# Kernel optimization log

Measured on AMD Instinct MI355X. Metric: run time of the kernel, lower is better.

Reference implementation:

```python
import jax, jax.numpy as jnp
import numpy as np

N = 100000
E = 3200000
IN_C = 128
HID = 128
OUT_C = 1


def setup_inputs() -> dict:
    key = jax.random.key(0)
    ks = jax.random.split(key, 12)
    x = jax.random.normal(ks[0], (N, IN_C), dtype=jnp.float32)
    edge_index = jax.random.randint(ks[1], (2, E), 0, N, dtype=jnp.int64)
    # GCNConv weights (PyG: lin(x) then aggregate, plus bias)
    s1 = 1.0 / np.sqrt(IN_C)
    s2 = 1.0 / np.sqrt(HID)
    W1 = jax.random.uniform(ks[2], (IN_C, HID), jnp.float32, -s1, s1)
    b1 = jnp.zeros((HID,), jnp.float32)
    W2 = jax.random.uniform(ks[3], (HID, HID), jnp.float32, -s2, s2)
    b2 = jnp.zeros((HID,), jnp.float32)
    sl1 = 1.0 / np.sqrt(2 * HID + IN_C)
    Wl1 = jax.random.uniform(ks[4], (2 * HID + IN_C, HID), jnp.float32, -sl1, sl1)
    bl1 = jax.random.uniform(ks[5], (HID,), jnp.float32, -sl1, sl1)
    Wl2 = jax.random.uniform(ks[6], (HID, OUT_C), jnp.float32, -s2, s2)
    bl2 = jax.random.uniform(ks[7], (OUT_C,), jnp.float32, -s2, s2)
    return {"x": x, "edge_index": edge_index, "W1": W1, "b1": b1,
            "W2": W2, "b2": b2, "Wl1": Wl1, "bl1": bl1, "Wl2": Wl2, "bl2": bl2}


def _gcn_conv(x, W, b, row, col, deg_inv_sqrt):
    # GCNConv: D^{-1/2} (A + I) D^{-1/2} X W + b  (self-loops added with weight 1)
    xw = x @ W                                   # [N, H]
    norm = deg_inv_sqrt[row] * deg_inv_sqrt[col] # [E]
    msg = xw[row] * norm[:, None]                # gather + scale
    agg = jax.ops.segment_sum(msg, col, num_segments=x.shape[0])  # scatter-add
    agg = agg + xw * (deg_inv_sqrt * deg_inv_sqrt)[:, None]       # self-loop term
    return agg + b


def reference(x, edge_index, W1, b1, W2, b2, Wl1, bl1, Wl2, bl2):
    row, col = edge_index[0], edge_index[1]  # source -> target
    n = x.shape[0]
    # degree with self-loops (edge weight 1)
    deg = jax.ops.segment_sum(jnp.ones_like(col, dtype=x.dtype), col, num_segments=n) + 1.0
    deg_inv_sqrt = jax.lax.rsqrt(deg)
    x1 = jax.nn.relu(_gcn_conv(x, W1, b1, row, col, deg_inv_sqrt))
    # dropout is identity in eval mode
    x2 = jax.nn.relu(_gcn_conv(x1, W2, b2, row, col, deg_inv_sqrt))
    h = jnp.concatenate([x, x1, x2], axis=-1)   # [N, in + 2*hidden]
    h = jax.nn.relu(h @ Wl1 + bl1)
    out = jax.nn.sigmoid(h @ Wl2 + bl2)         # [N, 1]
    return out
```

## Files before the change

kernel.cpp:

```cpp
#include <hip/hip_runtime.h>
#include <hip/hip_fp16.h>
#include <math.h>


typedef __attribute__((ext_vector_type(8))) short bf16x8;
typedef __attribute__((ext_vector_type(4))) float f32x4;

#define BSHIFT 5
#define NB 64
#define MAXBUK 4096

__global__ __launch_bounds__(1024) void k_bhist(const int* __restrict__ col,
                                                int* __restrict__ partials,
                                                int nbuk, int e) {
    __shared__ int h[MAXBUK];
    int tid = threadIdx.x;
    for (int i = tid; i < nbuk; i += 1024) h[i] = 0;
    __syncthreads();
    for (long long i = (long long)blockIdx.x * 1024 + tid; i < e;
         i += (long long)NB * 1024)
        atomicAdd(&h[col[i] >> BSHIFT], 1);
    __syncthreads();
    for (int i = tid; i < nbuk; i += 1024)
        partials[(size_t)blockIdx.x * nbuk + i] = h[i];
}

__global__ __launch_bounds__(256) void k_bscan(int* __restrict__ partials,
                                               int* __restrict__ tot, int nbuk) {
    int gid = blockIdx.x * 256 + threadIdx.x;
    int w = gid >> 6, l = gid & 63;
    if (w >= nbuk) return;
    size_t idx = (size_t)l * nbuk + w;
    int v = partials[idx];
    int s = v;
    for (int d = 1; d < 64; d <<= 1) {
        int t = __shfl_up(s, d);
        if (l >= d) s += t;
    }
    partials[idx] = s - v;
    if (l == 63) tot[w] = s;
}

__global__ __launch_bounds__(256) void k_btot(const int* __restrict__ tot,
                                              int* __restrict__ base,
                                              int nbuk, int e) {
    __shared__ int s[256];
    __shared__ int carry_s;
    int t = threadIdx.x;
    if (t == 0) carry_s = 0;
    __syncthreads();
    for (int bb = 0; bb < nbuk; bb += 256) {
        int v = (bb + t < nbuk) ? tot[bb + t] : 0;
        s[t] = v;
        __syncthreads();
        for (int d = 1; d < 256; d <<= 1) {
            int a = (t >= d) ? s[t - d] : 0;
            __syncthreads();
            s[t] += a;
            __syncthreads();
        }
        int c0 = carry_s;
        if (bb + t < nbuk) base[bb + t] = s[t] - v + c0;
        __syncthreads();
        if (t == 0) carry_s = c0 + s[255];
        __syncthreads();
    }
    if (t == 0) base[nbuk] = e;
}

__global__ __launch_bounds__(1024) void k_bscatter(
    const int* __restrict__ row, const int* __restrict__ col,
    const int* __restrict__ base, const int* __restrict__ partials,
    int* __restrict__ bpack, int nbuk, int e) {
    __shared__ int cur[MAXBUK];
    int tid = threadIdx.x;
    for (int i = tid; i < nbuk; i += 1024)
        cur[i] = base[i] + partials[(size_t)blockIdx.x * nbuk + i];
    __syncthreads();
    for (long long i = (long long)blockIdx.x * 1024 + tid; i < e;
         i += (long long)NB * 1024) {
        int c = col[i];
        int pos = atomicAdd(&cur[c >> BSHIFT], 1);
        bpack[pos] = (row[i] << BSHIFT) | (c & 31);
    }
}

__global__ __launch_bounds__(256) void k_bfill(
    const int* __restrict__ bpack, const int* __restrict__ base,
    int* __restrict__ offs, int* __restrict__ srow,
    float* __restrict__ dinv, int n, int e, int nbuk) {
    __shared__ int h[32];
    __shared__ int cur[32];
    int b = blockIdx.x, tid = threadIdx.x;
    int nodeb = b << BSHIFT;
    if (tid < 32) h[tid] = 0;
    __syncthreads();
    int s0 = base[b], s1 = base[b + 1];
    for (int i = s0 + tid; i < s1; i += 256) atomicAdd(&h[bpack[i] & 31], 1);
    __syncthreads();
    if (tid < 32) {
        int v = h[tid];
        int s = v;
        for (int d = 1; d < 32; d <<= 1) {
            int t = __shfl_up(s, d);
            if (tid >= d) s += t;
        }
        int myoff = s0 + s - v;
        cur[tid] = myoff;
        int node = nodeb + tid;
        if (node < n) {
            offs[node] = myoff;
            dinv[node] = rsqrtf((float)v + 1.0f);
        }
    }
    if (b == nbuk - 1 && tid == 0) offs[n] = e;
    __syncthreads();
    for (int i = s0 + tid; i < s1; i += 256) {
        int p = bpack[i];
        int pos = atomicAdd(&cur[p & 31], 1);
        srow[pos] = p >> BSHIFT;
    }
}

__global__ void k_prep_w(const float* __restrict__ W1, const float* __restrict__ W2,
                         const float* __restrict__ Wl1, short* __restrict__ wb) {
    int i = blockIdx.x * blockDim.x + threadIdx.x;
    if (i >= 5 * 16384) return;
    int blk = i >> 14, rem = i & 16383;
    int k = rem >> 7, n = rem & 127;
    float v;
    if (blk == 0) v = W1[rem];
    else if (blk == 1) v = W2[rem];
    else v = Wl1[((blk - 2) * 128 + k) * 128 + n];
    unsigned u = __float_as_uint(v);
    unsigned hb = u & 0xFFFF0000u;
    float lo = v - __uint_as_float(hb);
    unsigned lb = __float_as_uint(lo);
    int kk = k >> 5, km = k & 31;
    int half = km >> 4, kq = km & 15, g = kq >> 2, j = kq & 3;
    int nt = n >> 4, c = n & 15;
    size_t idx = ((size_t)(kk * 8 + nt) * 64 + (g * 16 + c)) * 8 + (half * 4 + j);
    size_t base = (size_t)blk * 32768;
    wb[base + idx] = (short)(hb >> 16);
    wb[base + 16384 + idx] = (short)(lb >> 16);
}

__device__ inline short2 split_f(float x) {
    unsigned u = __float_as_uint(x);
    unsigned hb = u & 0xFFFF0000u;
    short h = (short)(u >> 16);
    short l = (short)(__float_as_uint(x - __uint_as_float(hb)) >> 16);
    return make_short2(h, l);
}

__global__ __launch_bounds__(256) void k_gemm_mfma(
    const float* __restrict__ src0, const float* __restrict__ src1,
    const float* __restrict__ src2, const short* __restrict__ wb,
    const float* __restrict__ dscale, const float* __restrict__ bias,
    const float* __restrict__ wl2, const float* __restrict__ bl2,
    void* __restrict__ Y, int n, int nkb, int mode) {
    __shared__ short wl[32768];
    int tid = threadIdx.x;
    int wave = tid >> 6, lane = tid & 63;
    int g = lane >> 4, c = lane & 15;
    int base = blockIdx.x * 128 + wave * 32;

    f32x4 acc[2][8];
#pragma unroll
    for (int a = 0; a < 2; ++a)
#pragma unroll
        for (int b = 0; b < 8; ++b) acc[a][b] = (f32x4){0.f, 0.f, 0.f, 0.f};

    for (int kb = 0; kb < nkb; ++kb) {
        const float* src = (kb == 0) ? src0 : ((kb == 1) ? src1 : src2);
        __syncthreads();
        {
            const int4* s = (const int4*)(wb + (size_t)kb * 32768);
            int4* d = (int4*)wl;
            for (int it = tid; it < 4096; it += 256) d[it] = s[it];
        }
        __syncthreads();
#pragma unroll
        for (int kk = 0; kk < 4; ++kk) {
            bf16x8 ah[2], al[2];
#pragma unroll
            for (int mf = 0; mf < 2; ++mf) {
                int node = base + mf * 16 + c;
                if (node >= n) node = n - 1;
                const float* p = src + (size_t)node * 128 + kk * 32 + g * 4;
                float4 v0 = *(const float4*)p;
                float4 v1 = *(const float4*)(p + 16);
                short2 s;
                s = split_f(v0.x); ah[mf][0] = s.x; al[mf][0] = s.y;
                s = split_f(v0.y); ah[mf][1] = s.x; al[mf][1] = s.y;
                s = split_f(v0.z); ah[mf][2] = s.x; al[mf][2] = s.y;
                s = split_f(v0.w); ah[mf][3] = s.x; al[mf][3] = s.y;
                s = split_f(v1.x); ah[mf][4] = s.x; al[mf][4] = s.y;
                s = split_f(v1.y); ah[mf][5] = s.x; al[mf][5] = s.y;
                s = split_f(v1.z); ah[mf][6] = s.x; al[mf][6] = s.y;
                s = split_f(v1.w); ah[mf][7] = s.x; al[mf][7] = s.y;
            }
#pragma unroll
            for (int nt = 0; nt < 8; ++nt) {
                int bidx = ((kk * 8 + nt) * 64 + lane) * 8;
                bf16x8 bh = *(const bf16x8*)&wl[bidx];
                bf16x8 bl = *(const bf16x8*)&wl[16384 + bidx];
#pragma unroll
                for (int mf = 0; mf < 2; ++mf) {
                    acc[mf][nt] = __builtin_amdgcn_mfma_f32_16x16x32_bf16(ah[mf], bh, acc[mf][nt], 0, 0, 0);
                    acc[mf][nt] = __builtin_amdgcn_mfma_f32_16x16x32_bf16(ah[mf], bl, acc[mf][nt], 0, 0, 0);
                    acc[mf][nt] = __builtin_amdgcn_mfma_f32_16x16x32_bf16(al[mf], bh, acc[mf][nt], 0, 0, 0);
                }
            }
        }
    }

    if (mode == 0) {
        __half* Yh = (__half*)Y;
#pragma unroll
        for (int mf = 0; mf < 2; ++mf) {
#pragma unroll
            for (int j = 0; j < 4; ++j) {
                int node = base + mf * 16 + g * 4 + j;
                if (node >= n) continue;
                float s = dscale[node];
#pragma unroll
                for (int nt = 0; nt < 8; ++nt)
                    Yh[(size_t)node * 128 + nt * 16 + c] =
                        __float2half(acc[mf][nt][j] * s);
            }
        }
    } else {
        float* Yf = (float*)Y;
        float wv[8], bv[8];
#pragma unroll
        for (int nt = 0; nt < 8; ++nt) {
            wv[nt] = wl2[nt * 16 + c];
            bv[nt] = bias[nt * 16 + c];
        }
        float blv = bl2[0];
#pragma unroll
        for (int mf = 0; mf < 2; ++mf) {
#pragma unroll
            for (int j = 0; j < 4; ++j) {
                float partial = 0.f;
#pragma unroll
                for (int nt = 0; nt < 8; ++nt)
                    partial += fmaxf(acc[mf][nt][j] + bv[nt], 0.f) * wv[nt];
#pragma unroll
                for (int m = 1; m < 16; m <<= 1) partial += __shfl_xor(partial, m);
                int node = base + mf * 16 + g * 4 + j;
                if (c == 0 && node < n)
                    Yf[node] = 1.f / (1.f + expf(-(partial + blv)));
            }
        }
    }
}

__global__ __launch_bounds__(256) void k_aggregate(
    const __half* __restrict__ xws, const float* __restrict__ dinv,
    const float* __restrict__ bias, const int* __restrict__ offs,
    const int* __restrict__ srow, float* __restrict__ out, int n) {
    long long t = (long long)blockIdx.x * blockDim.x + threadIdx.x;
    int node = (int)(t >> 6);
    int l = (int)t & 63;
    if (node >= n) return;
    int start = offs[node], end = offs[node + 1];
    const __half* xb = xws + l * 2;
    float2 acc = __half22float2(*(const __half2*)(xb + (size_t)node * 128));
    int e = start;
    for (; e + 7 < end; e += 8) {
        int r0 = srow[e],     r1 = srow[e + 1], r2 = srow[e + 2], r3 = srow[e + 3];
        int r4 = srow[e + 4], r5 = srow[e + 5], r6 = srow[e + 6], r7 = srow[e + 7];
        float2 v0 = __half22float2(*(const __half2*)(xb + (size_t)r0 * 128));
        float2 v1 = __half22float2(*(const __half2*)(xb + (size_t)r1 * 128));
        float2 v2 = __half22float2(*(const __half2*)(xb + (size_t)r2 * 128));
        float2 v3 = __half22float2(*(const __half2*)(xb + (size_t)r3 * 128));
        float2 v4 = __half22float2(*(const __half2*)(xb + (size_t)r4 * 128));
        float2 v5 = __half22float2(*(const __half2*)(xb + (size_t)r5 * 128));
        float2 v6 = __half22float2(*(const __half2*)(xb + (size_t)r6 * 128));
        float2 v7 = __half22float2(*(const __half2*)(xb + (size_t)r7 * 128));
        acc.x += ((v0.x + v1.x) + (v2.x + v3.x)) + ((v4.x + v5.x) + (v6.x + v7.x));
        acc.y += ((v0.y + v1.y) + (v2.y + v3.y)) + ((v4.y + v5.y) + (v6.y + v7.y));
    }
    for (; e < end; ++e) {
        float2 v = __half22float2(*(const __half2*)(xb + (size_t)srow[e] * 128));
        acc.x += v.x;
        acc.y += v.y;
    }
    float s = dinv[node];
    float2 b = *(const float2*)(bias + l * 2);
    acc.x = fmaxf(fmaf(acc.x, s, b.x), 0.f);
    acc.y = fmaxf(fmaf(acc.y, s, b.y), 0.f);
    *(float2*)(out + (size_t)node * 128 + l * 2) = acc;
}

extern "C" void kernel_launch(void* const* d_in, const int* in_sizes, int n_in,
                              void* d_out, int out_size, void* d_ws, size_t ws_size,
                              hipStream_t stream) {
    const float* x   = (const float*)d_in[0];
    const int*   ei  = (const int*)d_in[1];
    const float* W1  = (const float*)d_in[2];
    const float* b1  = (const float*)d_in[3];
    const float* W2  = (const float*)d_in[4];
    const float* b2  = (const float*)d_in[5];
    const float* Wl1 = (const float*)d_in[6];
    const float* bl1 = (const float*)d_in[7];
    const float* Wl2 = (const float*)d_in[8];
    const float* bl2 = (const float*)d_in[9];
    float* out = (float*)d_out;

    const int N = in_sizes[0] / 128;
    const int E = in_sizes[1] / 2;
    const int* row = ei;
    const int* col = ei + E;
    const int nbuk = (N + 31) >> 5;

    char* ws = (char*)d_ws;
    size_t off = 0;
    auto alloc = [&](size_t bytes) {
        void* p = ws + off;
        off += (bytes + 255) & ~(size_t)255;
        return p;
    };
    float*  dinv     = (float*)alloc((size_t)N * 4);
    int*    partials = (int*)alloc((size_t)NB * nbuk * 4);
    int*    tot      = (int*)alloc((size_t)nbuk * 4);
    int*    base     = (int*)alloc((size_t)(nbuk + 1) * 4);
    int*    offs     = (int*)alloc((size_t)(N + 1) * 4);
    int*    bpack    = (int*)alloc((size_t)E * 4);
    int*    srow     = (int*)alloc((size_t)E * 4);
    short*  wb       = (short*)alloc((size_t)5 * 32768 * 2);
    __half* bufA     = (__half*)alloc((size_t)N * 128 * 2);
    float*  bufB     = (float*)alloc((size_t)N * 128 * 4);
    float*  bufC     = (float*)alloc((size_t)N * 128 * 4);

    const int B = 256;
    int gG = (N + 127) / 128;
    int gP = (5 * 16384 + B - 1) / B;
    int gS = (nbuk * 64 + B - 1) / B;
    int gA = (int)(((long long)N * 64 + B - 1) / B);

    k_prep_w<<<gP, B, 0, stream>>>(W1, W2, Wl1, wb);
    k_bhist<<<NB, 1024, 0, stream>>>(col, partials, nbuk, E);
    k_bscan<<<gS, B, 0, stream>>>(partials, tot, nbuk);
    k_btot<<<1, B, 0, stream>>>(tot, base, nbuk, E);
    k_bscatter<<<NB, 1024, 0, stream>>>(row, col, base, partials, bpack, nbuk, E);
    k_bfill<<<nbuk, B, 0, stream>>>(bpack, base, offs, srow, dinv, N, E, nbuk);

    k_gemm_mfma<<<gG, B, 0, stream>>>(x, nullptr, nullptr, wb,
                                      dinv, nullptr, nullptr, nullptr,
                                      bufA, N, 1, 0);
    k_aggregate<<<gA, B, 0, stream>>>(bufA, dinv, b1, offs, srow, bufB, N);

    k_gemm_mfma<<<gG, B, 0, stream>>>(bufB, nullptr, nullptr, wb + 32768,
                                      dinv, nullptr, nullptr, nullptr,
                                      bufA, N, 1, 0);
    k_aggregate<<<gA, B, 0, stream>>>(bufA, dinv, b2, offs, srow, bufC, N);

    k_gemm_mfma<<<gG, B, 0, stream>>>(x, bufB, bufC, wb + 2 * 32768,
                                      nullptr, bl1, Wl2, bl2,
                                      out, N, 3, 1);
}
```

Measured before the change: 470.3 us.

## Store hidden activations x1,x2 in fp16 and unroll aggregation by 16

```diff
diff --git a/kernel.cpp b/kernel.cpp
--- a/kernel.cpp
+++ b/kernel.cpp
@@ -153,12 +153,34 @@
     return make_short2(h, l);
 }
 
+__device__ inline void loadA8(const void* src, int f16, size_t node, int off,
+                              float* v) {
+    if (f16) {
+        const __half* p = (const __half*)src + node * 128 + off;
+        int2 a = *(const int2*)p;
+        int2 b = *(const int2*)(p + 16);
+        const __half2* ah = (const __half2*)&a;
+        const __half2* bh = (const __half2*)&b;
+        float2 f;
+        f = __half22float2(ah[0]); v[0] = f.x; v[1] = f.y;
+        f = __half22float2(ah[1]); v[2] = f.x; v[3] = f.y;
+        f = __half22float2(bh[0]); v[4] = f.x; v[5] = f.y;
+        f = __half22float2(bh[1]); v[6] = f.x; v[7] = f.y;
+    } else {
+        const float* p = (const float*)src + node * 128 + off;
+        float4 v0 = *(const float4*)p;
+        float4 v1 = *(const float4*)(p + 16);
+        v[0] = v0.x; v[1] = v0.y; v[2] = v0.z; v[3] = v0.w;
+        v[4] = v1.x; v[5] = v1.y; v[6] = v1.z; v[7] = v1.w;
+    }
+}
+
 __global__ __launch_bounds__(256) void k_gemm_mfma(
-    const float* __restrict__ src0, const float* __restrict__ src1,
-    const float* __restrict__ src2, const short* __restrict__ wb,
+    const void* __restrict__ src0, const void* __restrict__ src1,
+    const void* __restrict__ src2, const short* __restrict__ wb,
     const float* __restrict__ dscale, const float* __restrict__ bias,
     const float* __restrict__ wl2, const float* __restrict__ bl2,
-    void* __restrict__ Y, int n, int nkb, int mode) {
+    void* __restrict__ Y, int n, int nkb, int mode, int f16mask) {
     __shared__ short wl[32768];
     int tid = threadIdx.x;
     int wave = tid >> 6, lane = tid & 63;
@@ -172,7 +194,8 @@
         for (int b = 0; b < 8; ++b) acc[a][b] = (f32x4){0.f, 0.f, 0.f, 0.f};
 
     for (int kb = 0; kb < nkb; ++kb) {
-        const float* src = (kb == 0) ? src0 : ((kb == 1) ? src1 : src2);
+        const void* src = (kb == 0) ? src0 : ((kb == 1) ? src1 : src2);
+        int f16 = (f16mask >> kb) & 1;
         __syncthreads();
         {
             const int4* s = (const int4*)(wb + (size_t)kb * 32768);
@@ -187,18 +210,15 @@
             for (int mf = 0; mf < 2; ++mf) {
                 int node = base + mf * 16 + c;
                 if (node >= n) node = n - 1;
-                const float* p = src + (size_t)node * 128 + kk * 32 + g * 4;
-                float4 v0 = *(const float4*)p;
-                float4 v1 = *(const float4*)(p + 16);
+                float v[8];
+                loadA8(src, f16, (size_t)node, kk * 32 + g * 4, v);
                 short2 s;
-                s = split_f(v0.x); ah[mf][0] = s.x; al[mf][0] = s.y;
-                s = split_f(v0.y); ah[mf][1] = s.x; al[mf][1] = s.y;
-                s = split_f(v0.z); ah[mf][2] = s.x; al[mf][2] = s.y;
-                s = split_f(v0.w); ah[mf][3] = s.x; al[mf][3] = s.y;
-                s = split_f(v1.x); ah[mf][4] = s.x; al[mf][4] = s.y;
-                s = split_f(v1.y); ah[mf][5] = s.x; al[mf][5] = s.y;
-                s = split_f(v1.z); ah[mf][6] = s.x; al[mf][6] = s.y;
-                s = split_f(v1.w); ah[mf][7] = s.x; al[mf][7] = s.y;
+#pragma unroll
+                for (int q = 0; q < 8; ++q) {
+                    s = split_f(v[q]);
+                    ah[mf][q] = s.x;
+                    al[mf][q] = s.y;
+                }
             }
 #pragma unroll
             for (int nt = 0; nt < 8; ++nt) {
@@ -260,7 +280,7 @@
 __global__ __launch_bounds__(256) void k_aggregate(
     const __half* __restrict__ xws, const float* __restrict__ dinv,
     const float* __restrict__ bias, const int* __restrict__ offs,
-    const int* __restrict__ srow, float* __restrict__ out, int n) {
+    const int* __restrict__ srow, __half* __restrict__ out, int n) {
     long long t = (long long)blockIdx.x * blockDim.x + threadIdx.x;
     int node = (int)(t >> 6);
     int l = (int)t & 63;
@@ -269,19 +289,33 @@
     const __half* xb = xws + l * 2;
     float2 acc = __half22float2(*(const __half2*)(xb + (size_t)node * 128));
     int e = start;
+    for (; e + 15 < end; e += 16) {
+        int r[16];
+#pragma unroll
+        for (int q = 0; q < 16; ++q) r[q] = srow[e + q];
+        float2 v[16];
+#pragma unroll
+        for (int q = 0; q < 16; ++q)
+            v[q] = __half22float2(*(const __half2*)(xb + (size_t)r[q] * 128));
+        float sx = 0.f, sy = 0.f;
+#pragma unroll
+        for (int q = 0; q < 16; ++q) { sx += v[q].x; sy += v[q].y; }
+        acc.x += sx;
+        acc.y += sy;
+    }
     for (; e + 7 < end; e += 8) {
-        int r0 = srow[e],     r1 = srow[e + 1], r2 = srow[e + 2], r3 = srow[e + 3];
-        int r4 = srow[e + 4], r5 = srow[e + 5], r6 = srow[e + 6], r7 = srow[e + 7];
-        float2 v0 = __half22float2(*(const __half2*)(xb + (size_t)r0 * 128));
-        float2 v1 = __half22float2(*(const __half2*)(xb + (size_t)r1 * 128));
-        float2 v2 = __half22float2(*(const __half2*)(xb + (size_t)r2 * 128));
-        float2 v3 = __half22float2(*(const __half2*)(xb + (size_t)r3 * 128));
-        float2 v4 = __half22float2(*(const __half2*)(xb + (size_t)r4 * 128));
-        float2 v5 = __half22float2(*(const __half2*)(xb + (size_t)r5 * 128));
-        float2 v6 = __half22float2(*(const __half2*)(xb + (size_t)r6 * 128));
-        float2 v7 = __half22float2(*(const __half2*)(xb + (size_t)r7 * 128));
-        acc.x += ((v0.x + v1.x) + (v2.x + v3.x)) + ((v4.x + v5.x) + (v6.x + v7.x));
-        acc.y += ((v0.y + v1.y) + (v2.y + v3.y)) + ((v4.y + v5.y) + (v6.y + v7.y));
+        int r[8];
+#pragma unroll
+        for (int q = 0; q < 8; ++q) r[q] = srow[e + q];
+        float2 v[8];
+#pragma unroll
+        for (int q = 0; q < 8; ++q)
+            v[q] = __half22float2(*(const __half2*)(xb + (size_t)r[q] * 128));
+        float sx = 0.f, sy = 0.f;
+#pragma unroll
+        for (int q = 0; q < 8; ++q) { sx += v[q].x; sy += v[q].y; }
+        acc.x += sx;
+        acc.y += sy;
     }
     for (; e < end; ++e) {
         float2 v = __half22float2(*(const __half2*)(xb + (size_t)srow[e] * 128));
@@ -292,7 +326,7 @@
     float2 b = *(const float2*)(bias + l * 2);
     acc.x = fmaxf(fmaf(acc.x, s, b.x), 0.f);
     acc.y = fmaxf(fmaf(acc.y, s, b.y), 0.f);
-    *(float2*)(out + (size_t)node * 128 + l * 2) = acc;
+    *(__half2*)(out + (size_t)node * 128 + l * 2) = __float22half2_rn(acc);
 }
 
 extern "C" void kernel_launch(void* const* d_in, const int* in_sizes, int n_in,
@@ -332,8 +366,8 @@
     int*    srow     = (int*)alloc((size_t)E * 4);
     short*  wb       = (short*)alloc((size_t)5 * 32768 * 2);
     __half* bufA     = (__half*)alloc((size_t)N * 128 * 2);
-    float*  bufB     = (float*)alloc((size_t)N * 128 * 4);
-    float*  bufC     = (float*)alloc((size_t)N * 128 * 4);
+    __half* bufB     = (__half*)alloc((size_t)N * 128 * 2);
+    __half* bufC     = (__half*)alloc((size_t)N * 128 * 2);
 
     const int B = 256;
     int gG = (N + 127) / 128;
@@ -350,15 +384,15 @@
 
     k_gemm_mfma<<<gG, B, 0, stream>>>(x, nullptr, nullptr, wb,
                                       dinv, nullptr, nullptr, nullptr,
-                                      bufA, N, 1, 0);
+                                      bufA, N, 1, 0, 0);
     k_aggregate<<<gA, B, 0, stream>>>(bufA, dinv, b1, offs, srow, bufB, N);
 
     k_gemm_mfma<<<gG, B, 0, stream>>>(bufB, nullptr, nullptr, wb + 32768,
                                       dinv, nullptr, nullptr, nullptr,
-                                      bufA, N, 1, 0);
+                                      bufA, N, 1, 0, 1);
     k_aggregate<<<gA, B, 0, stream>>>(bufA, dinv, b2, offs, srow, bufC, N);
 
     k_gemm_mfma<<<gG, B, 0, stream>>>(x, bufB, bufC, wb + 2 * 32768,
                                       nullptr, bl1, Wl2, bl2,
-                                      out, N, 3, 1);
-}
+                                      out, N, 3, 1, 6);
+}
```

New measurement: 452.1 us. 3.9% less time.
